# Kernel optimization log

Measured on AMD Instinct MI355X. Metric: run time of the kernel, lower is better.

## Reference

```python
import jax, jax.numpy as jnp
import numpy as np
import math

EPS = 1e-6
N_LAYERS = 4
H = 48
PL = 4 * H  # params per layer (dense variant)
INV = math.log(math.exp(1.0 - EPS) - 1.0)
LOG100 = math.log(100.0)
B, S = 64, 256


def _logc(x):
    # torch: log(x*100)/ - log(100) trick for numerical behavior parity
    return jnp.log(x * 100.0) - LOG100


def _logsig(x):
    # DenseSigmoidFlow uses -softplus(-x) + EPS
    return -jax.nn.softplus(-x) + EPS


def _dense_layer(u_, w_, dsp, x, logdet, in_dim, h):
    # dsp: [B,S,4h], x: [B,in_or_prev_out], logdet: [B,S',out_prev,1] (or [B,1,1,1])
    pre_u = u_[None, None] + dsp[:, :, -in_dim:][:, :, None, :]          # [B,S,h,in]
    pre_w = w_[None, None] + dsp[:, :, 2 * h:3 * h][:, :, None, :]       # [B,S,out,h]
    a = jax.nn.softplus(dsp[:, :, 0:h] + INV) + EPS                       # [B,S,h]
    b = dsp[:, :, h:2 * h]                                                # [B,S,h]
    w = jax.nn.softmax(pre_w, axis=-1)
    u = jax.nn.softmax(pre_u, axis=-1)
    # broadcast-multiply-reduce over in_dim (x broadcasts against u's last dim)
    pre_sigm = jnp.sum(u * a[:, :, :, None] * x[:, None, None, :], axis=-1) + b  # [B,S,h]
    sigm = jax.nn.sigmoid(pre_sigm)
    x_pre = jnp.sum(w * sigm[:, :, None, :], axis=-1)                    # [B,S,out]
    xc = x_pre * (1.0 - EPS) + EPS * 0.5
    xnew = (_logc(xc) - _logc(1.0 - xc))[:, 0, :]                        # [B,out]
    logj = (jax.nn.log_softmax(pre_w, axis=-1)
            + _logsig(pre_sigm)[:, :, None, :]
            + _logsig(-pre_sigm)[:, :, None, :]
            + _logc(a)[:, :, None, :])                                   # [B,S,out,h]
    logj = logj[..., None] + jax.nn.log_softmax(pre_u, axis=-1)[:, :, None, :, :]  # [B,S,out,h,in]
    logj = jax.scipy.special.logsumexp(logj, axis=3)                     # [B,S,out,in]
    logdet_ = logj + math.log(1.0 - EPS) - (_logc(xc) + _logc(1.0 - xc))[:, :, :, None]
    logdet = jax.scipy.special.logsumexp(logdet_[..., None] + logdet[:, :, None, :, :], axis=3)  # [B,S,out,prev]
    return xnew, logdet


def setup_inputs() -> dict:
    key = jax.random.key(0)
    k1, k2, k3, k4, k5, k6 = jax.random.split(key, 6)
    params = jax.random.normal(k1, (B, S, N_LAYERS * PL), dtype=jnp.float32)
    x = jax.random.normal(k2, (B, 1), dtype=jnp.float32)
    lim = 1e-3
    u_mid = jax.random.uniform(k3, (N_LAYERS - 1, H, 1), minval=-lim, maxval=lim, dtype=jnp.float32)
    w_mid = jax.random.uniform(k4, (N_LAYERS - 1, H, H), minval=-lim, maxval=lim, dtype=jnp.float32)
    u_last = jax.random.uniform(k5, (H, H), minval=-lim, maxval=lim, dtype=jnp.float32)
    w_last = jax.random.uniform(k6, (1, H), minval=-lim, maxval=lim, dtype=jnp.float32)
    return {"params": params, "x": x, "u_mid": u_mid, "w_mid": w_mid,
            "u_last": u_last, "w_last": w_last}


def reference(params, x, u_mid, w_mid, u_last, w_last):
    logdet = jnp.zeros((x.shape[0], 1, 1, 1), dtype=x.dtype)
    for i in range(N_LAYERS):
        dsp = params[..., i * PL:(i + 1) * PL]
        if i < N_LAYERS - 1:
            x, logdet = _dense_layer(u_mid[i], w_mid[i], dsp, x, logdet, 1, H)
        else:
            x, logdet = _dense_layer(u_last, w_last, dsp, x, logdet, H, H)
    # final logdet is [B,S,1,1] -> flatten(start_dim=1) -> [B,S]
    return x, logdet.reshape(logdet.shape[0], -1)
```

## Files before the change

### kernel.cpp

```cpp
#include <hip/hip_runtime.h>
#include <math.h>
#include <stdint.h>

#define HH   48
#define RSW  25
#define MATW (HH*RSW)

#define EPSF     1e-6f
#define INVF     0.54132327f
#define LOG1MEPS (-1.0000005e-6f)

static __device__ __forceinline__ float fexp(float x){ return __expf(x); }
static __device__ __forceinline__ float flog(float x){ return __logf(x); }
static __device__ __forceinline__ float frcp(float x){
  float r = __builtin_amdgcn_rcpf(x);
  return r * (2.0f - x * r);
}
static __device__ __forceinline__ float wred_max(float v){
#pragma unroll
  for (int m = 32; m; m >>= 1) v = fmaxf(v, __shfl_xor(v, m, 64));
  return v;
}
static __device__ __forceinline__ float wred_sum(float v){
#pragma unroll
  for (int m = 32; m; m >>= 1) v += __shfl_xor(v, m, 64);
  return v;
}
static __device__ __forceinline__ float fsoftplus(float z){
  return fmaxf(z, 0.0f) + flog(1.0f + fexp(-fabsf(z)));
}
static __device__ __forceinline__ uint32_t bf16_rne(float x){
  uint32_t u = __float_as_uint(x);
  return (u + 0x7fffu + ((u >> 16) & 1u)) >> 16;
}
static __device__ __forceinline__ float bf_lo(uint32_t w){ return __uint_as_float(w << 16); }
static __device__ __forceinline__ float bf_hi(uint32_t w){ return __uint_as_float(w & 0xffff0000u); }

template<int NT>
static __device__ __forceinline__ void init_cmats(uint32_t* CW,
    const float* __restrict__ w_mid, const float* __restrict__ u_last, int tid){
  for (int w = tid; w < 4*HH*24; w += NT){
    int m   = w / (HH*24);
    int rem = w - m*(HH*24);
    int r   = rem / 24, t = rem - r*24;
    const float* src = (m < 3) ? (w_mid + m*HH*HH + r*HH + 2*t)
                               : (u_last + r*HH + 2*t);
    uint32_t b0 = bf16_rne(fexp(src[0]) - 1.0f);
    uint32_t b1 = bf16_rne(fexp(src[1]) - 1.0f);
    CW[m*MATW + r*RSW + t] = b0 | (b1 << 16);
  }
}

__global__ __launch_bounds__(256) void dsf_xchain(
    const float* __restrict__ params, const float* __restrict__ xin,
    const float* __restrict__ w_mid, const float* __restrict__ u_last,
    const float* __restrict__ w_last, float* __restrict__ ws,
    float* __restrict__ out_x)
{
  __shared__ uint32_t CW[4*MATW];
  __shared__ float4 pk[4][HH];

  init_cmats<256>(CW, w_mid, u_last, threadIdx.x);
  __syncthreads();

  const int wid  = threadIdx.x >> 6;
  const int lane = threadIdx.x & 63;
  const int b    = (blockIdx.x << 2) + wid;
  const bool act = lane < HH;
  const int jj   = act ? lane : (HH-1);
  const float* p = params + (size_t)b * 256 * 768;
  float4* mypk = pk[wid];

  float X  = xin[b];
  float xn = 0.0f;

#pragma unroll
  for (int L = 0; L < 3; ++L){
    const float* q = p + L*192;
    float d0 = q[jj], d1 = q[HH+jj], d2 = q[2*HH+jj];
    float a  = fsoftplus(d0 + INVF) + EPSF;
    float ps = fmaf(a, X, d1);
    float sg = frcp(1.0f + fexp(fminf(-ps, 88.0f)));
    float e  = act ? fexp(d2) : 0.0f;
    float E0 = wred_sum(e);
    float E1 = wred_sum(e * sg);
    if (act) mypk[lane] = make_float4(e, e*sg, 0.0f, 0.0f);
    __syncthreads();
    float t0 = E0, t1 = E1;
    const uint32_t* Cr = CW + L*MATW + jj*RSW;
#pragma unroll
    for (int t = 0; t < 24; ++t){
      uint32_t cw = Cr[t];
      float c0 = bf_lo(cw), c1 = bf_hi(cw);
      float4 q0 = mypk[2*t], q1 = mypk[2*t+1];
      t0 = fmaf(c0, q0.x, fmaf(c1, q1.x, t0));
      t1 = fmaf(c0, q0.y, fmaf(c1, q1.y, t1));
    }
    __syncthreads();
    float xp = fminf(fmaxf(t1 * frcp(t0), 0.0f), 1.0f);
    float xc = fmaf(xp, 1.0f - EPSF, 0.5f*EPSF);
    xn = flog(xc) - flog(1.0f - xc);
    if (L == 0){ X = wred_sum(act ? xn : 0.0f); if (lane == 0) ws[b] = X; }
    else if (L == 1){ X = wred_sum(act ? xn : 0.0f); if (lane == 0) ws[64 + b] = X; }
    else { if (act) ws[128 + b*HH + lane] = xn; }
  }

  const float* q = p + 3*192;
  float d0 = q[jj], d1 = q[HH+jj], d2 = q[2*HH+jj], d3 = q[3*HH+jj];
  float e3 = act ? fexp(d3) : 0.0f;
  float E30 = wred_sum(e3);
  float E31 = wred_sum(e3 * xn);
  if (act) mypk[lane] = make_float4(e3, e3*xn, 0.0f, 0.0f);
  __syncthreads();
  float s0 = E30, s1 = E31;
  const uint32_t* Ur = CW + 3*MATW + jj*RSW;
#pragma unroll
  for (int t = 0; t < 24; ++t){
    uint32_t cw = Ur[t];
    float c0 = bf_lo(cw), c1 = bf_hi(cw);
    float4 q0 = mypk[2*t], q1 = mypk[2*t+1];
    s0 = fmaf(c0, q0.x, fmaf(c1, q1.x, s0));
    s1 = fmaf(c0, q0.y, fmaf(c1, q1.y, s1));
  }
  float dotx = s1 * frcp(s0);
  float a  = fsoftplus(d0 + INVF) + EPSF;
  float ps = fmaf(a, dotx, d1);
  float sg = frcp(1.0f + fexp(fminf(-ps, 88.0f)));
  float pw = w_last[jj] + d2;
  float ew = act ? fexp(pw) : 0.0f;
  float Z  = wred_sum(ew);
  float xp = fminf(fmaxf(wred_sum(ew * sg) * frcp(Z), 0.0f), 1.0f);
  float xc = fmaf(xp, 1.0f - EPSF, 0.5f*EPSF);
  if (lane == 0) out_x[b] = flog(xc) - flog(1.0f - xc);
}

__global__ __launch_bounds__(256) void dsf_logdet(
    const float* __restrict__ params, const float* __restrict__ xin,
    const float* __restrict__ w_mid, const float* __restrict__ u_last,
    const float* __restrict__ w_last, const float* __restrict__ ws,
    float* __restrict__ out_ld)
{
  __shared__ uint32_t CW[4*MATW];
  __shared__ float4 pk[4][HH];
  __shared__ float wl[HH];

  init_cmats<256>(CW, w_mid, u_last, threadIdx.x);
  if (threadIdx.x < HH) wl[threadIdx.x] = w_last[threadIdx.x];
  __syncthreads();

  const int wid  = threadIdx.x >> 6;
  const int lane = threadIdx.x & 63;
  const int gw   = (blockIdx.x << 2) + wid;
  const int b    = gw >> 8;
  const bool act = lane < HH;
  const int jj   = act ? lane : (HH-1);
  const float* p = params + (size_t)gw * 768;
  float4* mypk = pk[wid];

  const float Xarr[3] = { xin[b], ws[b], ws[64 + b] };
  float ld = 0.0f;

#pragma unroll
  for (int L = 0; L < 3; ++L){
    const float* q = p + L*192;
    float d0 = q[jj], d1 = q[HH+jj], d2 = q[2*HH+jj];
    float a  = fsoftplus(d0 + INVF) + EPSF;
    float ps = fmaf(a, Xarr[L], d1);
    float sg = frcp(1.0f + fexp(fminf(-ps, 88.0f)));
    float ap = fabsf(ps);
    float S  = -ap - 2.0f*flog(1.0f + fexp(-ap)) + 2.0f*EPSF + flog(a);
    float Ms = wred_max(act ? (d2 + S) : -INFINITY);
    float e  = act ? fexp(d2) : 0.0f;
    float f2 = act ? fexp(d2 + S - Ms) : 0.0f;
    float E0 = wred_sum(e);
    float E1 = wred_sum(e * sg);
    float E2 = wred_sum(f2);
    if (act) mypk[lane] = make_float4(e, e*sg, f2, 0.0f);
    __syncthreads();
    float t0 = E0, t1 = E1, t2 = E2;
    const uint32_t* Cr = CW + L*MATW + jj*RSW;
#pragma unroll
    for (int t = 0; t < 24; ++t){
      uint32_t cw = Cr[t];
      float c0 = bf_lo(cw), c1 = bf_hi(cw);
      float4 q0 = mypk[2*t], q1 = mypk[2*t+1];
      t0 = fmaf(c0, q0.x, fmaf(c1, q1.x, t0));
      t1 = fmaf(c0, q0.y, fmaf(c1, q1.y, t1));
      t2 = fmaf(c0, q0.z, fmaf(c1, q1.z, t2));
    }
    __syncthreads();
    float xp  = fminf(fmaxf(t1 * frcp(t0), 0.0f), 1.0f);
    float xc  = fmaf(xp, 1.0f - EPSF, 0.5f*EPSF);
    float lxc = flog(xc), lxm = flog(1.0f - xc);
    float lj2 = Ms + flog(t2) - flog(t0);
    float lsep = 0.0f;
    if (L > 0){
      float mp = wred_max(act ? ld : -INFINITY);
      float sm = wred_sum(act ? fexp(ld - mp) : 0.0f);
      lsep = mp + flog(sm);
    }
    ld = lj2 + LOG1MEPS - lxc - lxm + lsep;
  }

  {
    const float* q = p + 3*192;
    float d0 = q[jj], d1 = q[HH+jj], d2 = q[2*HH+jj], d3 = q[3*HH+jj];
    float e3 = act ? fexp(d3) : 0.0f;
    float xv = ws[128 + b*HH + jj];
    float E30 = wred_sum(e3);
    float E31 = wred_sum(e3 * xv);
    if (act) mypk[lane] = make_float4(e3, e3*xv, 0.0f, 0.0f);
    __syncthreads();
    float s0 = E30, s1 = E31;
    const uint32_t* Ur = CW + 3*MATW + jj*RSW;
#pragma unroll
    for (int t = 0; t < 24; ++t){
      uint32_t cw = Ur[t];
      float c0 = bf_lo(cw), c1 = bf_hi(cw);
      float4 q0 = mypk[2*t], q1 = mypk[2*t+1];
      s0 = fmaf(c0, q0.x, fmaf(c1, q1.x, s0));
      s1 = fmaf(c0, q0.y, fmaf(c1, q1.y, s1));
    }
    float dotx = s1 * frcp(s0);
    float lseu = flog(s0);
    float a  = fsoftplus(d0 + INVF) + EPSF;
    float ps = fmaf(a, dotx, d1);
    float sg = frcp(1.0f + fexp(fminf(-ps, 88.0f)));
    float ap = fabsf(ps);
    float Sp = -ap - 2.0f*flog(1.0f + fexp(-ap)) + 2.0f*EPSF + flog(a);
    float pw = wl[jj] + d2;
    float ew = act ? fexp(pw) : 0.0f;
    float Z  = wred_sum(ew);
    float xp = fminf(fmaxf(wred_sum(ew * sg) * frcp(Z), 0.0f), 1.0f);
    float lsew = flog(Z);
    float xc  = fmaf(xp, 1.0f - EPSF, 0.5f*EPSF);
    float lxc = flog(xc), lxm = flog(1.0f - xc);
    float c  = (pw - lsew) + Sp - lseu;
    float Mc = wred_max(act ? c : -INFINITY);
    float ec = act ? fexp(c - Mc) : 0.0f;
    float Ec = wred_sum(ec);
    __syncthreads();
    if (act) mypk[lane].x = ec;
    __syncthreads();
    const uint32_t sh = (jj & 1) ? 0u : 16u;
    const int kw = jj >> 1;
    float acc = Ec;
#pragma unroll 8
    for (int j = 0; j < HH; ++j){
      uint32_t cw = CW[3*MATW + j*RSW + kw];
      float cc = __uint_as_float((cw << sh) & 0xffff0000u);
      acc = fmaf(mypk[j].x, cc, acc);
    }
    float lj2k = d3 + Mc + flog(acc);
    float tot  = act ? (lj2k + LOG1MEPS - lxc - lxm + ld) : -INFINITY;
    float Mt = wred_max(tot);
    float sm = wred_sum(act ? fexp(tot - Mt) : 0.0f);
    if (lane == 0) out_ld[gw] = Mt + flog(sm);
  }
}

extern "C" void kernel_launch(void* const* d_in, const int* in_sizes, int n_in,
                              void* d_out, int out_size, void* d_ws, size_t ws_size,
                              hipStream_t stream) {
  const float* params = (const float*)d_in[0];
  const float* xin    = (const float*)d_in[1];
  const float* w_mid  = (const float*)d_in[3];
  const float* u_last = (const float*)d_in[4];
  const float* w_last = (const float*)d_in[5];
  float* out = (float*)d_out;
  float* ws  = (float*)d_ws;

  hipLaunchKernelGGL(dsf_xchain, dim3(16), dim3(256), 0, stream,
                     params, xin, w_mid, u_last, w_last, ws, out);
  hipLaunchKernelGGL(dsf_logdet, dim3(4096), dim3(256), 0, stream,
                     params, xin, w_mid, u_last, w_last, ws, out + 64);
}
```

Baseline: 180.1 us.

## Drop block barriers, share exp in sigmoid/logsig, merge logs, use 512-thread blocks

Removes __syncthreads around the per-wave shared scratch, since each wave only touches its own pk slot and relies on wavefront lockstep. Computes the sigmoid and the log-sigmoid terms from a single exp(-|ps|) and merges pairs of logs into one. The logdet kernel now uses 512-thread blocks with half as many blocks, which halves the redundant per-block bf16 matrix table initialization. Without barriers, correctness depends on the compiler not reordering LDS writes and reads within a wave. Merging logs can lose precision when xc is near 0 or 1.

```diff
diff --git a/kernel.cpp b/kernel.cpp
--- a/kernel.cpp
+++ b/kernel.cpp
@@ -51,6 +51,8 @@
   }
 }
 
+#define SIGMOID_FROM_E(ps, E, R) ( ((ps) >= 0.0f) ? (R) : (E)*(R) )
+
 __global__ __launch_bounds__(256) void dsf_xchain(
     const float* __restrict__ params, const float* __restrict__ xin,
     const float* __restrict__ w_mid, const float* __restrict__ u_last,
@@ -80,12 +82,14 @@
     float d0 = q[jj], d1 = q[HH+jj], d2 = q[2*HH+jj];
     float a  = fsoftplus(d0 + INVF) + EPSF;
     float ps = fmaf(a, X, d1);
-    float sg = frcp(1.0f + fexp(fminf(-ps, 88.0f)));
+    float ap = fabsf(ps);
+    float E  = fexp(-ap);
+    float R  = frcp(1.0f + E);
+    float sg = SIGMOID_FROM_E(ps, E, R);
     float e  = act ? fexp(d2) : 0.0f;
     float E0 = wred_sum(e);
     float E1 = wred_sum(e * sg);
     if (act) mypk[lane] = make_float4(e, e*sg, 0.0f, 0.0f);
-    __syncthreads();
     float t0 = E0, t1 = E1;
     const uint32_t* Cr = CW + L*MATW + jj*RSW;
 #pragma unroll
@@ -96,10 +100,9 @@
       t0 = fmaf(c0, q0.x, fmaf(c1, q1.x, t0));
       t1 = fmaf(c0, q0.y, fmaf(c1, q1.y, t1));
     }
-    __syncthreads();
     float xp = fminf(fmaxf(t1 * frcp(t0), 0.0f), 1.0f);
     float xc = fmaf(xp, 1.0f - EPSF, 0.5f*EPSF);
-    xn = flog(xc) - flog(1.0f - xc);
+    xn = flog(xc * frcp(1.0f - xc));
     if (L == 0){ X = wred_sum(act ? xn : 0.0f); if (lane == 0) ws[b] = X; }
     else if (L == 1){ X = wred_sum(act ? xn : 0.0f); if (lane == 0) ws[64 + b] = X; }
     else { if (act) ws[128 + b*HH + lane] = xn; }
@@ -111,7 +114,6 @@
   float E30 = wred_sum(e3);
   float E31 = wred_sum(e3 * xn);
   if (act) mypk[lane] = make_float4(e3, e3*xn, 0.0f, 0.0f);
-  __syncthreads();
   float s0 = E30, s1 = E31;
   const uint32_t* Ur = CW + 3*MATW + jj*RSW;
 #pragma unroll
@@ -125,32 +127,35 @@
   float dotx = s1 * frcp(s0);
   float a  = fsoftplus(d0 + INVF) + EPSF;
   float ps = fmaf(a, dotx, d1);
-  float sg = frcp(1.0f + fexp(fminf(-ps, 88.0f)));
+  float ap = fabsf(ps);
+  float E  = fexp(-ap);
+  float R  = frcp(1.0f + E);
+  float sg = SIGMOID_FROM_E(ps, E, R);
   float pw = w_last[jj] + d2;
   float ew = act ? fexp(pw) : 0.0f;
   float Z  = wred_sum(ew);
   float xp = fminf(fmaxf(wred_sum(ew * sg) * frcp(Z), 0.0f), 1.0f);
   float xc = fmaf(xp, 1.0f - EPSF, 0.5f*EPSF);
-  if (lane == 0) out_x[b] = flog(xc) - flog(1.0f - xc);
-}
-
-__global__ __launch_bounds__(256) void dsf_logdet(
+  if (lane == 0) out_x[b] = flog(xc * frcp(1.0f - xc));
+}
+
+__global__ __launch_bounds__(512) void dsf_logdet(
     const float* __restrict__ params, const float* __restrict__ xin,
     const float* __restrict__ w_mid, const float* __restrict__ u_last,
     const float* __restrict__ w_last, const float* __restrict__ ws,
     float* __restrict__ out_ld)
 {
   __shared__ uint32_t CW[4*MATW];
-  __shared__ float4 pk[4][HH];
+  __shared__ float4 pk[8][HH];
   __shared__ float wl[HH];
 
-  init_cmats<256>(CW, w_mid, u_last, threadIdx.x);
+  init_cmats<512>(CW, w_mid, u_last, threadIdx.x);
   if (threadIdx.x < HH) wl[threadIdx.x] = w_last[threadIdx.x];
   __syncthreads();
 
   const int wid  = threadIdx.x >> 6;
   const int lane = threadIdx.x & 63;
-  const int gw   = (blockIdx.x << 2) + wid;
+  const int gw   = (blockIdx.x << 3) + wid;
   const int b    = gw >> 8;
   const bool act = lane < HH;
   const int jj   = act ? lane : (HH-1);
@@ -166,9 +171,11 @@
     float d0 = q[jj], d1 = q[HH+jj], d2 = q[2*HH+jj];
     float a  = fsoftplus(d0 + INVF) + EPSF;
     float ps = fmaf(a, Xarr[L], d1);
-    float sg = frcp(1.0f + fexp(fminf(-ps, 88.0f)));
     float ap = fabsf(ps);
-    float S  = -ap - 2.0f*flog(1.0f + fexp(-ap)) + 2.0f*EPSF + flog(a);
+    float E  = fexp(-ap);
+    float R  = frcp(1.0f + E);
+    float sg = SIGMOID_FROM_E(ps, E, R);
+    float S  = -ap - 2.0f*flog(1.0f + E) + 2.0f*EPSF + flog(a);
     float Ms = wred_max(act ? (d2 + S) : -INFINITY);
     float e  = act ? fexp(d2) : 0.0f;
     float f2 = act ? fexp(d2 + S - Ms) : 0.0f;
@@ -176,7 +183,6 @@
     float E1 = wred_sum(e * sg);
     float E2 = wred_sum(f2);
     if (act) mypk[lane] = make_float4(e, e*sg, f2, 0.0f);
-    __syncthreads();
     float t0 = E0, t1 = E1, t2 = E2;
     const uint32_t* Cr = CW + L*MATW + jj*RSW;
 #pragma unroll
@@ -188,18 +194,17 @@
       t1 = fmaf(c0, q0.y, fmaf(c1, q1.y, t1));
       t2 = fmaf(c0, q0.z, fmaf(c1, q1.z, t2));
     }
-    __syncthreads();
-    float xp  = fminf(fmaxf(t1 * frcp(t0), 0.0f), 1.0f);
-    float xc  = fmaf(xp, 1.0f - EPSF, 0.5f*EPSF);
-    float lxc = flog(xc), lxm = flog(1.0f - xc);
-    float lj2 = Ms + flog(t2) - flog(t0);
+    float xp   = fminf(fmaxf(t1 * frcp(t0), 0.0f), 1.0f);
+    float xc   = fmaf(xp, 1.0f - EPSF, 0.5f*EPSF);
+    float lsum = flog(xc * (1.0f - xc));
+    float lj2  = Ms + flog(t2 * frcp(t0));
     float lsep = 0.0f;
     if (L > 0){
       float mp = wred_max(act ? ld : -INFINITY);
       float sm = wred_sum(act ? fexp(ld - mp) : 0.0f);
       lsep = mp + flog(sm);
     }
-    ld = lj2 + LOG1MEPS - lxc - lxm + lsep;
+    ld = lj2 + LOG1MEPS - lsum + lsep;
   }
 
   {
@@ -210,7 +215,6 @@
     float E30 = wred_sum(e3);
     float E31 = wred_sum(e3 * xv);
     if (act) mypk[lane] = make_float4(e3, e3*xv, 0.0f, 0.0f);
-    __syncthreads();
     float s0 = E30, s1 = E31;
     const uint32_t* Ur = CW + 3*MATW + jj*RSW;
 #pragma unroll
@@ -225,23 +229,23 @@
     float lseu = flog(s0);
     float a  = fsoftplus(d0 + INVF) + EPSF;
     float ps = fmaf(a, dotx, d1);
-    float sg = frcp(1.0f + fexp(fminf(-ps, 88.0f)));
     float ap = fabsf(ps);
-    float Sp = -ap - 2.0f*flog(1.0f + fexp(-ap)) + 2.0f*EPSF + flog(a);
+    float E  = fexp(-ap);
+    float R  = frcp(1.0f + E);
+    float sg = SIGMOID_FROM_E(ps, E, R);
+    float Sp = -ap - 2.0f*flog(1.0f + E) + 2.0f*EPSF + flog(a);
     float pw = wl[jj] + d2;
     float ew = act ? fexp(pw) : 0.0f;
     float Z  = wred_sum(ew);
     float xp = fminf(fmaxf(wred_sum(ew * sg) * frcp(Z), 0.0f), 1.0f);
     float lsew = flog(Z);
-    float xc  = fmaf(xp, 1.0f - EPSF, 0.5f*EPSF);
-    float lxc = flog(xc), lxm = flog(1.0f - xc);
+    float xc   = fmaf(xp, 1.0f - EPSF, 0.5f*EPSF);
+    float lsum = flog(xc * (1.0f - xc));
     float c  = (pw - lsew) + Sp - lseu;
     float Mc = wred_max(act ? c : -INFINITY);
     float ec = act ? fexp(c - Mc) : 0.0f;
     float Ec = wred_sum(ec);
-    __syncthreads();
     if (act) mypk[lane].x = ec;
-    __syncthreads();
     const uint32_t sh = (jj & 1) ? 0u : 16u;
     const int kw = jj >> 1;
     float acc = Ec;
@@ -252,7 +256,7 @@
       acc = fmaf(mypk[j].x, cc, acc);
     }
     float lj2k = d3 + Mc + flog(acc);
-    float tot  = act ? (lj2k + LOG1MEPS - lxc - lxm + ld) : -INFINITY;
+    float tot  = act ? (lj2k + LOG1MEPS - lsum + ld) : -INFINITY;
     float Mt = wred_max(tot);
     float sm = wred_sum(act ? fexp(tot - Mt) : 0.0f);
     if (lane == 0) out_ld[gw] = Mt + flog(sm);
@@ -272,6 +276,6 @@
 
   hipLaunchKernelGGL(dsf_xchain, dim3(16), dim3(256), 0, stream,
                      params, xin, w_mid, u_last, w_last, ws, out);
-  hipLaunchKernelGGL(dsf_logdet, dim3(4096), dim3(256), 0, stream,
+  hipLaunchKernelGGL(dsf_logdet, dim3(2048), dim3(512), 0, stream,
                      params, xin, w_mid, u_last, w_last, ws, out + 64);
 }
```

Result: slower. 207.1 us (+15.0%).
